# Kernel optimization log

Measured on AMD Instinct MI355X. Metric: run time of the kernel, lower is better.

## Reference

```python
import jax, jax.numpy as jnp
import numpy as np

SEQ, DM, NH, DH = 8192, 1024, 16, 64


def setup_inputs() -> dict:
    key = jax.random.key(0)
    k = jax.random.split(key, 8)
    return {
        "xs": jax.random.normal(k[0], (SEQ, DM), dtype=jnp.float32),
        "wq": jax.random.normal(k[1], (NH, DH, DM), dtype=jnp.float32),
        "wk": jax.random.normal(k[2], (NH, DH, DM), dtype=jnp.float32),
        "wv": jax.random.normal(k[3], (NH, DH, DM), dtype=jnp.float32),
        # MLP: Linear(NH*DH -> DM), gelu, Linear(DM -> NH*DH); eqx stores W as (out, in)
        "w1": jax.random.normal(k[4], (DM, NH * DH), dtype=jnp.float32) * 0.02,
        "b1": jnp.zeros((DM,), dtype=jnp.float32),
        "w2": jax.random.normal(k[5], (NH * DH, DM), dtype=jnp.float32) * 0.02,
        "b2": jnp.zeros((NH * DH,), dtype=jnp.float32),
    }


def _act(x):
    return jax.nn.elu(x) + 1.0


def reference(xs, wq, wk, wv, w1, b1, w2, b2):
    # project: (n_heads d_head d_model),(seq d_model) -> (seq n_heads d_head)
    q = jnp.einsum('hdm,sm->shd', wq, xs)
    k = jnp.einsum('hdm,sm->shd', wk, xs)
    v = jnp.einsum('hdm,sm->shd', wv, xs)

    def cell(state, qkv):
        s, z = state                      # s: (h, dk, dv), z: (h, dk)
        qt, kt, vt = qkv                  # each (h, d)
        kt = _act(kt)
        s = s + jnp.einsum('hk,hv->hkv', kt, vt)
        z = z + kt
        qa = _act(qt)
        # faithful to einops 'n_heads d_head_k d_head_v, n_heads d_head_q -> n_heads d_head_v'
        sq = jnp.einsum('hkv,hq->hv', s, qa)
        zq = jnp.einsum('hk,hq->h', z, qa)
        return (s, z), sq / zq[:, None]

    init = (jnp.zeros((NH, DH, DH), xs.dtype), jnp.zeros((NH, DH), xs.dtype))
    _, out = jax.lax.scan(cell, init, (q, k, v))   # out: (seq, h, d)
    out = out.reshape(SEQ, NH * DH)
    h = jax.nn.gelu(out @ w1.T + b1)
    return h @ w2.T + b2
```

## Files before the change

kernel.cpp:

```cpp
#include <hip/hip_runtime.h>
#include <hip/hip_bf16.h>

using bf16 = __hip_bfloat16;
typedef __attribute__((ext_vector_type(8))) short shortx8;
typedef __attribute__((ext_vector_type(4))) float f32x4;

#define SEQ 8192
#define DM 1024
#define NH 16
#define CHUNK 64
#define NC (SEQ / CHUNK)
#define NT (DM / 64)

__device__ __forceinline__ void load_lds16(const bf16* g, bf16* l) {
    __builtin_amdgcn_global_load_lds(
        (const __attribute__((address_space(1))) void*)g,
        (__attribute__((address_space(3))) void*)l, 16, 0, 0);
}

__device__ __forceinline__ unsigned ldsoff(const bf16* p) {
    return (unsigned)(unsigned long long)(__attribute__((address_space(3))) const void*)p;
}

__device__ __forceinline__ shortx8 dsr128(unsigned a) {
    shortx8 r;
    asm volatile("ds_read_b128 %0, %1" : "=v"(r) : "v"(a));
    return r;
}

__device__ __forceinline__ float bf2f(short s) {
    union { unsigned u; float f; } x;
    x.u = ((unsigned)(unsigned short)s) << 16;
    return x.f;
}

__global__ __launch_bounds__(256) void convert_all(const float* __restrict__ xs,
                                                   const float* __restrict__ wk,
                                                   const float* __restrict__ wv,
                                                   const float* __restrict__ w1,
                                                   const float* __restrict__ w2,
                                                   bf16* __restrict__ xsb,
                                                   bf16* __restrict__ wall) {
    const int b = blockIdx.x;
    const float* in;
    bf16* out;
    int blk;
    if (b < 8192) {
        in = xs; out = xsb; blk = b;
    } else {
        const int seg = (b - 8192) >> 10;
        blk = (b - 8192) & 1023;
        out = wall + (size_t)seg * DM * DM;
        if (seg == 0)      in = wk;
        else if (seg == 1) in = wv;
        else if (seg == 2) in = w1;
        else               in = w2;
    }
    size_t i = ((size_t)blk * 256 + threadIdx.x) * 4;
    float4 f = *(const float4*)(in + i);
    out[i + 0] = __float2bfloat16(f.x);
    out[i + 1] = __float2bfloat16(f.y);
    out[i + 2] = __float2bfloat16(f.z);
    out[i + 3] = __float2bfloat16(f.w);
}

__global__ __launch_bounds__(512, 2) void gemm256(const bf16* __restrict__ A,
                                                  const bf16* __restrict__ B,
                                                  void* __restrict__ Cv,
                                                  float* __restrict__ kappa,
                                                  int N) {
    __shared__ __align__(16) bf16 As[2][256][64];
    __shared__ __align__(16) bf16 Bs[2][256][64];

    const int tid = threadIdx.x;
    const int nwg = gridDim.x * gridDim.y;
    const int bid = blockIdx.x + blockIdx.y * gridDim.x;
    const int cpx = nwg >> 3;
    const int swz = (bid & 7) * cpx + (bid >> 3);
    const int ry  = swz % gridDim.y;
    const int rx  = swz / gridDim.y;
    const int bm  = ry * 256;
    const int bn  = rx * 256;

    const int wave = tid >> 6;
    const int lane = tid & 63;
    const int wr   = wave >> 2;
    const int wc   = wave & 3;
    const int quad = lane >> 4;
    const int m16  = lane & 15;
    const int r7   = m16 & 7;
    const int wr128 = wr * 128;
    const int wc64  = wc * 64;
    const int kp0 = ((quad ^ r7) * 8);
    const int kp1 = (((4 + quad) ^ r7) * 8);

    auto stageA = [&](int half, int kt) {
        #pragma unroll
        for (int it = 0; it < 2; ++it) {
            int s = it * 512 + tid;
            int row = s >> 3, pos = s & 7;
            int g = pos ^ (row & 7);
            load_lds16(A + (size_t)(bm + half * 128 + row) * DM + kt * 64 + g * 8,
                       &As[kt & 1][half * 128 + row][pos * 8]);
        }
    };
    auto stageB = [&](int half, int kt) {
        #pragma unroll
        for (int it = 0; it < 2; ++it) {
            int s = it * 512 + tid;
            int row = s >> 3, pos = s & 7;
            int g = pos ^ (row & 7);
            load_lds16(B + (size_t)(bn + half * 128 + row) * DM + kt * 64 + g * 8,
                       &Bs[kt & 1][half * 128 + row][pos * 8]);
        }
    };

    f32x4 acc[8][4];
    #pragma unroll
    for (int i = 0; i < 8; ++i)
        #pragma unroll
        for (int j = 0; j < 4; ++j)
            #pragma unroll
            for (int r = 0; r < 4; ++r) acc[i][j][r] = 0.f;

    stageA(0, 0); stageA(1, 0); stageB(0, 0); stageB(1, 0);
    stageB(0, 1); stageB(1, 1);
    asm volatile("s_waitcnt vmcnt(4)");
    __builtin_amdgcn_s_barrier();

    shortx8 af[4][2], blo[2][2], bhi[2][2];

    #pragma unroll 1
    for (int t = 0; t < NT; ++t) {
        const int sl = t & 1;
        #pragma unroll
        for (int i = 0; i < 4; ++i) {
            af[i][0] = dsr128(ldsoff(&As[sl][wr128 + i * 16 + m16][kp0]));
            af[i][1] = dsr128(ldsoff(&As[sl][wr128 + i * 16 + m16][kp1]));
        }
        #pragma unroll
        for (int j = 0; j < 2; ++j) {
            blo[j][0] = dsr128(ldsoff(&Bs[sl][wc64 + j * 16 + m16][kp0]));
            blo[j][1] = dsr128(ldsoff(&Bs[sl][wc64 + j * 16 + m16][kp1]));
        }
        if (t + 1 < NT) stageA(0, t + 1);
        __builtin_amdgcn_s_barrier();
        asm volatile("s_waitcnt lgkmcnt(0)");
        __builtin_amdgcn_sched_barrier(0);
        __builtin_amdgcn_s_setprio(1);
        #pragma unroll
        for (int i = 0; i < 4; ++i)
            #pragma unroll
            for (int j = 0; j < 2; ++j) {
                acc[i][j] = __builtin_amdgcn_mfma_f32_16x16x32_bf16(af[i][0], blo[j][0], acc[i][j], 0, 0, 0);
                acc[i][j] = __builtin_amdgcn_mfma_f32_16x16x32_bf16(af[i][1], blo[j][1], acc[i][j], 0, 0, 0);
            }
        __builtin_amdgcn_s_setprio(0);
        __builtin_amdgcn_s_barrier();

        #pragma unroll
        for (int j = 0; j < 2; ++j) {
            bhi[j][0] = dsr128(ldsoff(&Bs[sl][wc64 + (j + 2) * 16 + m16][kp0]));
            bhi[j][1] = dsr128(ldsoff(&Bs[sl][wc64 + (j + 2) * 16 + m16][kp1]));
        }
        if (t + 1 < NT) stageA(1, t + 1);
        __builtin_amdgcn_s_barrier();
        asm volatile("s_waitcnt lgkmcnt(0)");
        __builtin_amdgcn_sched_barrier(0);
        __builtin_amdgcn_s_setprio(1);
        #pragma unroll
        for (int i = 0; i < 4; ++i)
            #pragma unroll
            for (int j = 0; j < 2; ++j) {
                acc[i][j + 2] = __builtin_amdgcn_mfma_f32_16x16x32_bf16(af[i][0], bhi[j][0], acc[i][j + 2], 0, 0, 0);
                acc[i][j + 2] = __builtin_amdgcn_mfma_f32_16x16x32_bf16(af[i][1], bhi[j][1], acc[i][j + 2], 0, 0, 0);
            }
        __builtin_amdgcn_s_setprio(0);
        __builtin_amdgcn_s_barrier();

        #pragma unroll
        for (int i = 0; i < 4; ++i) {
            af[i][0] = dsr128(ldsoff(&As[sl][wr128 + 64 + i * 16 + m16][kp0]));
            af[i][1] = dsr128(ldsoff(&As[sl][wr128 + 64 + i * 16 + m16][kp1]));
        }
        if (t + 2 < NT) stageB(0, t + 2);
        __builtin_amdgcn_s_barrier();
        asm volatile("s_waitcnt lgkmcnt(0)");
        __builtin_amdgcn_sched_barrier(0);
        __builtin_amdgcn_s_setprio(1);
        #pragma unroll
        for (int i = 0; i < 4; ++i)
            #pragma unroll
            for (int j = 0; j < 2; ++j) {
                acc[4 + i][j] = __builtin_amdgcn_mfma_f32_16x16x32_bf16(af[i][0], blo[j][0], acc[4 + i][j], 0, 0, 0);
                acc[4 + i][j] = __builtin_amdgcn_mfma_f32_16x16x32_bf16(af[i][1], blo[j][1], acc[4 + i][j], 0, 0, 0);
            }
        __builtin_amdgcn_s_setprio(0);
        __builtin_amdgcn_s_barrier();

        if (t + 2 < NT) {
            stageB(1, t + 2);
            asm volatile("s_waitcnt vmcnt(4)");
        } else {
            asm volatile("s_waitcnt vmcnt(0)");
        }
        __builtin_amdgcn_s_barrier();
        __builtin_amdgcn_s_setprio(1);
        #pragma unroll
        for (int i = 0; i < 4; ++i)
            #pragma unroll
            for (int j = 0; j < 2; ++j) {
                acc[4 + i][j + 2] = __builtin_amdgcn_mfma_f32_16x16x32_bf16(af[i][0], bhi[j][0], acc[4 + i][j + 2], 0, 0, 0);
                acc[4 + i][j + 2] = __builtin_amdgcn_mfma_f32_16x16x32_bf16(af[i][1], bhi[j][1], acc[4 + i][j + 2], 0, 0, 0);
            }
        __builtin_amdgcn_s_setprio(0);
        __builtin_amdgcn_s_barrier();
    }

    const int gcol0 = bn + wc64;
    if (gcol0 < DM) {
        const int h = gcol0 >> 6;
        #pragma unroll
        for (int i = 0; i < 8; ++i) {
            #pragma unroll
            for (int r = 0; r < 4; ++r) {
                float s = 0.f;
                #pragma unroll
                for (int j = 0; j < 4; ++j) {
                    float v = acc[i][j][r];
                    s += v > 0.f ? v + 1.f : __expf(v);
                }
                s += __shfl_xor(s, 1);
                s += __shfl_xor(s, 2);
                s += __shfl_xor(s, 4);
                s += __shfl_xor(s, 8);
                if (m16 == 0)
                    kappa[(size_t)h * SEQ + bm + wr128 + i * 16 + quad * 4 + r] = s;
            }
        }
    } else {
        bf16* vb = (bf16*)Cv;
        #pragma unroll
        for (int i = 0; i < 8; ++i) {
            int row0 = bm + wr128 + i * 16 + quad * 4;
            #pragma unroll
            for (int j = 0; j < 4; ++j) {
                int col = gcol0 - DM + j * 16 + m16;
                #pragma unroll
                for (int r = 0; r < 4; ++r)
                    vb[(size_t)(row0 + r) * DM + col] = __float2bfloat16(acc[i][j][r]);
            }
        }
    }
}

template <int MODE>
__global__ __launch_bounds__(512, 2) void gemm_mlp(const bf16* __restrict__ A,
                                                   const bf16* __restrict__ B,
                                                   void* __restrict__ Cv,
                                                   const float* __restrict__ bias,
                                                   int N) {
    __shared__ __align__(16) bf16 As[3][128][64];
    __shared__ __align__(16) bf16 Bs[2][256][64];

    const int tid = threadIdx.x;
    const int nwg = gridDim.x * gridDim.y;
    const int bid = blockIdx.x + blockIdx.y * gridDim.x;
    const int cpx = nwg >> 3;
    const int swz = (bid & 7) * cpx + (bid >> 3);
    const int ry  = swz % gridDim.y;
    const int rx  = swz / gridDim.y;
    const int bm  = ry * 128;
    const int bn  = rx * 256;

    const int wave = tid >> 6;
    const int lane = tid & 63;
    const int wr   = wave >> 2;
    const int wc   = wave & 3;
    const int quad = lane >> 4;
    const int m16  = lane & 15;
    const int r7   = m16 & 7;
    const int wr64 = wr * 64;
    const int wc64 = wc * 64;
    const int kp0 = ((quad ^ r7) * 8);
    const int kp1 = (((4 + quad) ^ r7) * 8);

    auto stageA = [&](int slot, int kt) {
        #pragma unroll
        for (int it = 0; it < 2; ++it) {
            int s = it * 512 + tid;
            int row = s >> 3, pos = s & 7;
            int g = pos ^ (row & 7);
            load_lds16(A + (size_t)(bm + row) * DM + kt * 64 + g * 8,
                       &As[slot][row][pos * 8]);
        }
    };
    auto stageB = [&](int half, int kt) {
        #pragma unroll
        for (int it = 0; it < 2; ++it) {
            int s = it * 512 + tid;
            int row = s >> 3, pos = s & 7;
            int g = pos ^ (row & 7);
            load_lds16(B + (size_t)(bn + half * 128 + row) * DM + kt * 64 + g * 8,
                       &Bs[kt & 1][half * 128 + row][pos * 8]);
        }
    };

    f32x4 acc[4][4];
    #pragma unroll
    for (int i = 0; i < 4; ++i)
        #pragma unroll
        for (int j = 0; j < 4; ++j)
            #pragma unroll
            for (int r = 0; r < 4; ++r) acc[i][j][r] = 0.f;

    stageA(0, 0); stageB(0, 0); stageB(1, 0);
    stageA(1, 1); stageB(0, 1); stageB(1, 1);
    asm volatile("s_waitcnt vmcnt(0)");
    __builtin_amdgcn_s_barrier();

    shortx8 af[4][2], bfr[4][2];

    int sl3 = 0;
    int st3 = 2;

    #pragma unroll 1
    for (int t = 0; t < NT; ++t) {
        const int slB = t & 1;
        if (t + 2 < NT) stageA(st3, t + 2);
        #pragma unroll
        for (int i = 0; i < 4; ++i) {
            af[i][0] = dsr128(ldsoff(&As[sl3][wr64 + i * 16 + m16][kp0]));
            af[i][1] = dsr128(ldsoff(&As[sl3][wr64 + i * 16 + m16][kp1]));
        }
        #pragma unroll
        for (int j = 0; j < 4; ++j) {
            bfr[j][0] = dsr128(ldsoff(&Bs[slB][wc64 + j * 16 + m16][kp0]));
            bfr[j][1] = dsr128(ldsoff(&Bs[slB][wc64 + j * 16 + m16][kp1]));
        }
        __builtin_amdgcn_s_barrier();
        asm volatile("s_waitcnt lgkmcnt(0)");
        __builtin_amdgcn_sched_barrier(0);
        __builtin_amdgcn_s_setprio(1);
        #pragma unroll
        for (int i = 0; i < 4; ++i)
            #pragma unroll
            for (int j = 0; j < 2; ++j) {
                acc[i][j] = __builtin_amdgcn_mfma_f32_16x16x32_bf16(af[i][0], bfr[j][0], acc[i][j], 0, 0, 0);
                acc[i][j] = __builtin_amdgcn_mfma_f32_16x16x32_bf16(af[i][1], bfr[j][1], acc[i][j], 0, 0, 0);
            }
        __builtin_amdgcn_s_setprio(0);
        __builtin_amdgcn_s_barrier();

        if (t + 2 < NT) {
            stageB(0, t + 2);
            stageB(1, t + 2);
            asm volatile("s_waitcnt vmcnt(6)");
        } else {
            asm volatile("s_waitcnt vmcnt(0)");
        }
        __builtin_amdgcn_s_barrier();
        __builtin_amdgcn_s_setprio(1);
        #pragma unroll
        for (int i = 0; i < 4; ++i)
            #pragma unroll
            for (int j = 0; j < 2; ++j) {
                acc[i][j + 2] = __builtin_amdgcn_mfma_f32_16x16x32_bf16(af[i][0], bfr[j + 2][0], acc[i][j + 2], 0, 0, 0);
                acc[i][j + 2] = __builtin_amdgcn_mfma_f32_16x16x32_bf16(af[i][1], bfr[j + 2][1], acc[i][j + 2], 0, 0, 0);
            }
        __builtin_amdgcn_s_setprio(0);
        sl3 = (sl3 == 2) ? 0 : sl3 + 1;
        st3 = (st3 == 2) ? 0 : st3 + 1;
    }

    #pragma unroll
    for (int i = 0; i < 4; ++i) {
        int row0 = bm + wr64 + i * 16 + quad * 4;
        #pragma unroll
        for (int j = 0; j < 4; ++j) {
            int col = bn + wc64 + j * 16 + m16;
            float bv = bias[col];
            #pragma unroll
            for (int r = 0; r < 4; ++r) {
                float v = acc[i][j][r] + bv;
                if (MODE == 2) {
                    float tt = tanhf(0.7978845608028654f * (v + 0.044715f * v * v * v));
                    ((bf16*)Cv)[(size_t)(row0 + r) * N + col] = __float2bfloat16(0.5f * v * (1.f + tt));
                } else {
                    ((float*)Cv)[(size_t)(row0 + r) * N + col] = v;
                }
            }
        }
    }
}

__global__ __launch_bounds__(256) void chunk_sums(const bf16* __restrict__ vb,
                                                  const float* __restrict__ kappa,
                                                  float* __restrict__ numbuf,
                                                  float* __restrict__ denbuf) {
    const int h = blockIdx.x, c = blockIdx.y;
    const int v = threadIdx.x & 63, tq = threadIdx.x >> 6;
    __shared__ float red[4][64];
    __shared__ float dred[4];
    float np = 0.f, dp = 0.f;
    #pragma unroll
    for (int i = 0; i < 16; ++i) {
        int t = c * 64 + tq * 16 + i;
        float kv = kappa[(size_t)h * SEQ + t];
        float vv = bf2f(((const short*)vb)[(size_t)t * DM + h * 64 + v]);
        np += kv * vv;
        dp += kv;
    }
    red[tq][v] = np;
    if (v == 0) dred[tq] = dp;
    __syncthreads();
    if (tq == 0) {
        float s = red[0][v] + red[1][v] + red[2][v] + red[3][v];
        numbuf[((size_t)h * NC + c) * 64 + v] = s;
        if (v == 0)
            denbuf[(size_t)h * NC + c] = dred[0] + dred[1] + dred[2] + dred[3];
    }
}

__global__ __launch_bounds__(256) void prefix_state(float* __restrict__ numbuf,
                                                    float* __restrict__ denbuf) {
    const int h = blockIdx.x;
    const int wave = threadIdx.x >> 6;
    const int d = threadIdx.x & 63;
    __shared__ float tot[4][64];
    __shared__ float dtot[4];

    float val[32], dval[32];
    const int c0 = wave * 32;
    #pragma unroll
    for (int i = 0; i < 32; ++i) {
        size_t idx = (size_t)h * NC + c0 + i;
        val[i]  = numbuf[idx * 64 + d];
        dval[i] = denbuf[idx];
    }
    float run = 0.f, drun = 0.f;
    #pragma unroll
    for (int i = 0; i < 32; ++i) {
        float t = val[i];  val[i]  = run;  run  += t;
        float dt = dval[i]; dval[i] = drun; drun += dt;
    }
    tot[wave][d] = run;
    if (d == 0) dtot[wave] = drun;
    __syncthreads();
    float off = 0.f, doff = 0.f;
    for (int w = 0; w < wave; ++w) { off += tot[w][d]; doff += dtot[w]; }
    #pragma unroll
    for (int i = 0; i < 32; ++i) {
        size_t idx = (size_t)h * NC + c0 + i;
        numbuf[idx * 64 + d] = val[i] + off;
        if (d == 0) denbuf[idx] = dval[i] + doff;
    }
}

__global__ __launch_bounds__(256) void chunk_out(const bf16* __restrict__ vb,
                                                 const float* __restrict__ kappa,
                                                 const float* __restrict__ numbuf,
                                                 const float* __restrict__ denbuf,
                                                 bf16* __restrict__ out) {
    const int h = blockIdx.x, c = blockIdx.y;
    __shared__ float Ksh[64];
    __shared__ float Vs[64][64];
    const int tid = threadIdx.x;

    #pragma unroll
    for (int it = 0; it < 2; ++it) {
        int s = it * 256 + tid;
        int r = s >> 3, d8 = (s & 7) * 8;
        shortx8 raw = *(const shortx8*)(vb + (size_t)(c * 64 + r) * DM + h * 64 + d8);
        #pragma unroll
        for (int e = 0; e < 8; ++e) Vs[r][d8 + e] = bf2f(raw[e]);
    }
    if (tid < 64) Ksh[tid] = kappa[(size_t)h * SEQ + c * 64 + tid];
    __syncthreads();

    const int t  = tid >> 2;
    const int v0 = (tid & 3) << 4;
    const size_t bidx = (size_t)h * NC + c;

    float den = denbuf[bidx];
    float num[16];
    #pragma unroll
    for (int jj = 0; jj < 4; ++jj) {
        float4 n4 = *(const float4*)&numbuf[bidx * 64 + v0 + jj * 4];
        num[jj * 4 + 0] = n4.x; num[jj * 4 + 1] = n4.y;
        num[jj * 4 + 2] = n4.z; num[jj * 4 + 3] = n4.w;
    }

    for (int i = 0; i <= t; ++i) {
        float s = Ksh[i];
        den += s;
        #pragma unroll
        for (int jj = 0; jj < 4; ++jj) {
            float4 v4 = *(const float4*)&Vs[i][v0 + jj * 4];
            num[jj * 4 + 0] += s * v4.x; num[jj * 4 + 1] += s * v4.y;
            num[jj * 4 + 2] += s * v4.z; num[jj * 4 + 3] += s * v4.w;
        }
    }

    const float inv = 1.0f / den;
    size_t og = (size_t)(c * 64 + t) * DM + h * 64 + v0;
    #pragma unroll
    for (int j = 0; j < 16; ++j) out[og + j] = __float2bfloat16(num[j] * inv);
}

extern "C" void kernel_launch(void* const* d_in, const int* in_sizes, int n_in,
                              void* d_out, int out_size, void* d_ws, size_t ws_size,
                              hipStream_t stream) {
    const float* xs = (const float*)d_in[0];
    const float* wk = (const float*)d_in[2];
    const float* wv = (const float*)d_in[3];
    const float* w1 = (const float*)d_in[4];
    const float* b1 = (const float*)d_in[5];
    const float* w2 = (const float*)d_in[6];
    const float* b2 = (const float*)d_in[7];
    float* y = (float*)d_out;

    char* base = (char*)d_ws;
    size_t off = 0;
    auto alloc = [&](size_t b) -> char* {
        char* p = base + off;
        off += (b + 255) & ~(size_t)255;
        return p;
    };

    const size_t NMAT = (size_t)SEQ * DM;
    const size_t NW   = (size_t)DM * DM;
    bf16*  xsb    = (bf16*)alloc(NMAT * 2);
    bf16*  wall   = (bf16*)alloc(4 * NW * 2);
    bf16*  w1b    = wall + 2 * NW;
    bf16*  w2b    = wall + 3 * NW;
    bf16*  vb     = (bf16*)alloc(NMAT * 2);
    float* kappa  = (float*)alloc((size_t)NH * SEQ * 4);
    float* numbuf = (float*)alloc((size_t)NH * NC * 64 * 4);
    float* denbuf = (float*)alloc((size_t)NH * NC * 4);
    bf16*  outb   = (bf16*)alloc(NMAT * 2);
    bf16*  hb     = (bf16*)alloc(NMAT * 2);

    convert_all<<<8192 + 4 * 1024, 256, 0, stream>>>(xs, wk, wv, w1, w2,
                                                     xsb, wall);

    gemm256<<<dim3(2048 / 256, SEQ / 256), 512, 0, stream>>>(
        xsb, wall, vb, kappa, 2048);

    chunk_sums<<<dim3(NH, NC), 256, 0, stream>>>(vb, kappa, numbuf, denbuf);
    prefix_state<<<NH, 256, 0, stream>>>(numbuf, denbuf);
    chunk_out<<<dim3(NH, NC), 256, 0, stream>>>(vb, kappa, numbuf, denbuf, outb);

    gemm_mlp<2><<<dim3(DM / 256, SEQ / 128), 512, 0, stream>>>(
        outb, w1b, hb, b1, DM);
    gemm_mlp<3><<<dim3(DM / 256, SEQ / 128), 512, 0, stream>>>(
        hb, w2b, y, b2, DM);
}
```

Baseline: 215.9 us.

## Restructure GEMM main loops into fewer phases with fewer barriers

The QKV projection GEMM loop goes from four MFMA phases per k-tile, each fenced by two barriers, to two larger phases. Each phase does more LDS reads and MFMAs, and the A and B global-to-LDS prefetches are issued earlier. The MLP GEMM drops a barrier, issues its B prefetch before the second MFMA half, and relaxes the prologue wait to vmcnt(6). This is meant to cut barrier stalls and improve overlap, at the cost of more live fragment registers and a higher risk of LDS read/write races.

```diff
diff --git a/kernel.cpp b/kernel.cpp
--- a/kernel.cpp
+++ b/kernel.cpp
@@ -133,6 +133,7 @@
     #pragma unroll 1
     for (int t = 0; t < NT; ++t) {
         const int sl = t & 1;
+        if (t + 1 < NT) { stageA(0, t + 1); stageA(1, t + 1); }
         #pragma unroll
         for (int i = 0; i < 4; ++i) {
             af[i][0] = dsr128(ldsoff(&As[sl][wr128 + i * 16 + m16][kp0]));
@@ -142,9 +143,9 @@
         for (int j = 0; j < 2; ++j) {
             blo[j][0] = dsr128(ldsoff(&Bs[sl][wc64 + j * 16 + m16][kp0]));
             blo[j][1] = dsr128(ldsoff(&Bs[sl][wc64 + j * 16 + m16][kp1]));
-        }
-        if (t + 1 < NT) stageA(0, t + 1);
-        __builtin_amdgcn_s_barrier();
+            bhi[j][0] = dsr128(ldsoff(&Bs[sl][wc64 + (j + 2) * 16 + m16][kp0]));
+            bhi[j][1] = dsr128(ldsoff(&Bs[sl][wc64 + (j + 2) * 16 + m16][kp1]));
+        }
         asm volatile("s_waitcnt lgkmcnt(0)");
         __builtin_amdgcn_sched_barrier(0);
         __builtin_amdgcn_s_setprio(1);
@@ -154,17 +155,18 @@
             for (int j = 0; j < 2; ++j) {
                 acc[i][j] = __builtin_amdgcn_mfma_f32_16x16x32_bf16(af[i][0], blo[j][0], acc[i][j], 0, 0, 0);
                 acc[i][j] = __builtin_amdgcn_mfma_f32_16x16x32_bf16(af[i][1], blo[j][1], acc[i][j], 0, 0, 0);
+                acc[i][j + 2] = __builtin_amdgcn_mfma_f32_16x16x32_bf16(af[i][0], bhi[j][0], acc[i][j + 2], 0, 0, 0);
+                acc[i][j + 2] = __builtin_amdgcn_mfma_f32_16x16x32_bf16(af[i][1], bhi[j][1], acc[i][j + 2], 0, 0, 0);
             }
         __builtin_amdgcn_s_setprio(0);
         __builtin_amdgcn_s_barrier();
 
-        #pragma unroll
-        for (int j = 0; j < 2; ++j) {
-            bhi[j][0] = dsr128(ldsoff(&Bs[sl][wc64 + (j + 2) * 16 + m16][kp0]));
-            bhi[j][1] = dsr128(ldsoff(&Bs[sl][wc64 + (j + 2) * 16 + m16][kp1]));
-        }
-        if (t + 1 < NT) stageA(1, t + 1);
-        __builtin_amdgcn_s_barrier();
+        if (t + 2 < NT) { stageB(0, t + 2); stageB(1, t + 2); }
+        #pragma unroll
+        for (int i = 0; i < 4; ++i) {
+            af[i][0] = dsr128(ldsoff(&As[sl][wr128 + 64 + i * 16 + m16][kp0]));
+            af[i][1] = dsr128(ldsoff(&As[sl][wr128 + 64 + i * 16 + m16][kp1]));
+        }
         asm volatile("s_waitcnt lgkmcnt(0)");
         __builtin_amdgcn_sched_barrier(0);
         __builtin_amdgcn_s_setprio(1);
@@ -172,48 +174,17 @@
         for (int i = 0; i < 4; ++i)
             #pragma unroll
             for (int j = 0; j < 2; ++j) {
-                acc[i][j + 2] = __builtin_amdgcn_mfma_f32_16x16x32_bf16(af[i][0], bhi[j][0], acc[i][j + 2], 0, 0, 0);
-                acc[i][j + 2] = __builtin_amdgcn_mfma_f32_16x16x32_bf16(af[i][1], bhi[j][1], acc[i][j + 2], 0, 0, 0);
-            }
-        __builtin_amdgcn_s_setprio(0);
-        __builtin_amdgcn_s_barrier();
-
-        #pragma unroll
-        for (int i = 0; i < 4; ++i) {
-            af[i][0] = dsr128(ldsoff(&As[sl][wr128 + 64 + i * 16 + m16][kp0]));
-            af[i][1] = dsr128(ldsoff(&As[sl][wr128 + 64 + i * 16 + m16][kp1]));
-        }
-        if (t + 2 < NT) stageB(0, t + 2);
-        __builtin_amdgcn_s_barrier();
-        asm volatile("s_waitcnt lgkmcnt(0)");
-        __builtin_amdgcn_sched_barrier(0);
-        __builtin_amdgcn_s_setprio(1);
-        #pragma unroll
-        for (int i = 0; i < 4; ++i)
-            #pragma unroll
-            for (int j = 0; j < 2; ++j) {
                 acc[4 + i][j] = __builtin_amdgcn_mfma_f32_16x16x32_bf16(af[i][0], blo[j][0], acc[4 + i][j], 0, 0, 0);
                 acc[4 + i][j] = __builtin_amdgcn_mfma_f32_16x16x32_bf16(af[i][1], blo[j][1], acc[4 + i][j], 0, 0, 0);
+                acc[4 + i][j + 2] = __builtin_amdgcn_mfma_f32_16x16x32_bf16(af[i][0], bhi[j][0], acc[4 + i][j + 2], 0, 0, 0);
+                acc[4 + i][j + 2] = __builtin_amdgcn_mfma_f32_16x16x32_bf16(af[i][1], bhi[j][1], acc[4 + i][j + 2], 0, 0, 0);
             }
         __builtin_amdgcn_s_setprio(0);
-        __builtin_amdgcn_s_barrier();
-
         if (t + 2 < NT) {
-            stageB(1, t + 2);
             asm volatile("s_waitcnt vmcnt(4)");
         } else {
             asm volatile("s_waitcnt vmcnt(0)");
         }
-        __builtin_amdgcn_s_barrier();
-        __builtin_amdgcn_s_setprio(1);
-        #pragma unroll
-        for (int i = 0; i < 4; ++i)
-            #pragma unroll
-            for (int j = 0; j < 2; ++j) {
-                acc[4 + i][j + 2] = __builtin_amdgcn_mfma_f32_16x16x32_bf16(af[i][0], bhi[j][0], acc[4 + i][j + 2], 0, 0, 0);
-                acc[4 + i][j + 2] = __builtin_amdgcn_mfma_f32_16x16x32_bf16(af[i][1], bhi[j][1], acc[4 + i][j + 2], 0, 0, 0);
-            }
-        __builtin_amdgcn_s_setprio(0);
         __builtin_amdgcn_s_barrier();
     }
 
@@ -316,7 +287,7 @@
 
     stageA(0, 0); stageB(0, 0); stageB(1, 0);
     stageA(1, 1); stageB(0, 1); stageB(1, 1);
-    asm volatile("s_waitcnt vmcnt(0)");
+    asm volatile("s_waitcnt vmcnt(6)");
     __builtin_amdgcn_s_barrier();
 
     shortx8 af[4][2], bfr[4][2];
@@ -338,7 +309,6 @@
             bfr[j][0] = dsr128(ldsoff(&Bs[slB][wc64 + j * 16 + m16][kp0]));
             bfr[j][1] = dsr128(ldsoff(&Bs[slB][wc64 + j * 16 + m16][kp1]));
         }
-        __builtin_amdgcn_s_barrier();
         asm volatile("s_waitcnt lgkmcnt(0)");
         __builtin_amdgcn_sched_barrier(0);
         __builtin_amdgcn_s_setprio(1);
@@ -352,23 +322,22 @@
         __builtin_amdgcn_s_setprio(0);
         __builtin_amdgcn_s_barrier();
 
+        if (t + 2 < NT) { stageB(0, t + 2); stageB(1, t + 2); }
+        __builtin_amdgcn_s_setprio(1);
+        #pragma unroll
+        for (int i = 0; i < 4; ++i)
+            #pragma unroll
+            for (int j = 0; j < 2; ++j) {
+                acc[i][j + 2] = __builtin_amdgcn_mfma_f32_16x16x32_bf16(af[i][0], bfr[j + 2][0], acc[i][j + 2], 0, 0, 0);
+                acc[i][j + 2] = __builtin_amdgcn_mfma_f32_16x16x32_bf16(af[i][1], bfr[j + 2][1], acc[i][j + 2], 0, 0, 0);
+            }
+        __builtin_amdgcn_s_setprio(0);
         if (t + 2 < NT) {
-            stageB(0, t + 2);
-            stageB(1, t + 2);
             asm volatile("s_waitcnt vmcnt(6)");
         } else {
             asm volatile("s_waitcnt vmcnt(0)");
         }
         __builtin_amdgcn_s_barrier();
-        __builtin_amdgcn_s_setprio(1);
-        #pragma unroll
-        for (int i = 0; i < 4; ++i)
-            #pragma unroll
-            for (int j = 0; j < 2; ++j) {
-                acc[i][j + 2] = __builtin_amdgcn_mfma_f32_16x16x32_bf16(af[i][0], bfr[j + 2][0], acc[i][j + 2], 0, 0, 0);
-                acc[i][j + 2] = __builtin_amdgcn_mfma_f32_16x16x32_bf16(af[i][1], bfr[j + 2][1], acc[i][j + 2], 0, 0, 0);
-            }
-        __builtin_amdgcn_s_setprio(0);
         sl3 = (sl3 == 2) ? 0 : sl3 + 1;
         st3 = (st3 == 2) ? 0 : st3 + 1;
     }
```

Result: no change. 215.4 us (-0.3%).
